# Performance work log

Measured on AMD Instinct MI355X. Metric: run time of the kernel, lower is better.

Reference implementation:

```python
import jax, jax.numpy as jnp
import numpy as np

T, B, E, H = 4096, 1, 256, 8
D = E // H  # head_dim = 32


def setup_inputs() -> dict:
    root = jax.random.key(0)
    ks = jax.random.split(root, 12)
    s = 0.02
    return {
        "query": jax.random.normal(ks[0], (T, B, E), dtype=jnp.float32),
        "key": jax.random.normal(ks[1], (T, B, E), dtype=jnp.float32),
        "value": jax.random.normal(ks[2], (T, B, E), dtype=jnp.float32),
        "residual_attn": jax.random.normal(ks[3], (H, T, T), dtype=jnp.float32),
        "Wq": jax.random.normal(ks[4], (E, E), dtype=jnp.float32) * s,
        "bq": jnp.zeros((E,), dtype=jnp.float32),
        "Wk": jax.random.normal(ks[5], (E, E), dtype=jnp.float32) * s,
        "bk": jnp.zeros((E,), dtype=jnp.float32),
        "Wv": jax.random.normal(ks[6], (E, E), dtype=jnp.float32) * s,
        "bv": jnp.zeros((E,), dtype=jnp.float32),
        "Wo": jax.random.normal(ks[7], (E, E), dtype=jnp.float32) * s,
        "bo": jnp.zeros((E,), dtype=jnp.float32),
    }


def reference(query, key, value, residual_attn, Wq, bq, Wk, bk, Wv, bv, Wo, bo):
    t, b, e = query.shape
    h = H
    d = e // h
    scaling = d ** (-0.5)
    # Original forward: `query = key = self.with_pos_embed(query, pos)` with pos=None,
    # so both q and k are projected from `query`; the `key` arg is ignored.
    qk_src = query
    q = (qk_src @ Wq.T + bq) * scaling          # [T, B, E]
    k = qk_src @ Wk.T + bk                       # [T, B, E]
    v = value @ Wv.T + bv                        # [T, B, E]

    def split_heads(x):
        # [T, B, E] -> [B, H, T, D]
        return x.reshape(t, b, h, d).transpose(1, 2, 0, 3)

    qh, kh, vh = split_heads(q), split_heads(k), split_heads(v)
    # scores: [B, H, T, S] with residual attention added pre-softmax
    scores = jnp.einsum('bhtd,bhsd->bhts', qh, kh) + residual_attn[None]
    attn = jax.nn.softmax(scores, axis=-1)       # dropout p=0.0 -> no-op
    out = jnp.einsum('bhts,bhsd->bhtd', attn, vh)  # [B, H, T, D]
    out = out.transpose(2, 0, 1, 3).reshape(t, b, e)  # [T, B, E]
    return out @ Wo.T + bo
```

## Files before the change

### kernel.cpp

```cpp
#include <hip/hip_runtime.h>
#include <hip/hip_bf16.h>

#define T_DIM 4096
#define E_DIM 256
#define H_DIM 8
#define D_DIM 32
#define SSPLIT 2

typedef __attribute__((ext_vector_type(8))) short short8;
typedef __attribute__((ext_vector_type(4))) float f32x4;

__device__ __forceinline__ unsigned short f2bf(float f) {
    union { float f; unsigned u; } x; x.f = f;
    return (unsigned short)((x.u + 0x7FFFu + ((x.u >> 16) & 1u)) >> 16);
}

struct CastArgs {
    const float* src[6];
    unsigned short* dst[6];
    int n4[6];
};

__global__ __launch_bounds__(256) void cast_kernel(CastArgs a) {
    int b = blockIdx.y;
    const float* s = a.src[b];
    unsigned short* d = a.dst[b];
    int n4 = a.n4[b];
    int i = blockIdx.x * 256 + threadIdx.x;
    if (i < n4) {
        float4 v = reinterpret_cast<const float4*>(s)[i];
        ushort4 o;
        o.x = f2bf(v.x); o.y = f2bf(v.y); o.z = f2bf(v.z); o.w = f2bf(v.w);
        reinterpret_cast<ushort4*>(d)[i] = o;
    }
}

__global__ __launch_bounds__(256) void proj_kernel(
    const unsigned short* __restrict__ qb, const unsigned short* __restrict__ vb,
    const unsigned short* __restrict__ wq, const unsigned short* __restrict__ wk,
    const unsigned short* __restrict__ wv,
    const float* __restrict__ bq, const float* __restrict__ bk, const float* __restrict__ bv,
    unsigned short* __restrict__ qw, unsigned short* __restrict__ kw,
    unsigned short* __restrict__ vt)
{
    const int z = blockIdx.z;
    const unsigned short* A = (z == 2) ? vb : qb;
    const unsigned short* W = (z == 0) ? wq : (z == 1) ? wk : wv;
    const float* bias = (z == 0) ? bq : (z == 1) ? bk : bv;

    const int tid = threadIdx.x;
    const int w = tid >> 6, lane = tid & 63;
    const int g = lane >> 4, r = lane & 15;
    const int t0 = blockIdx.x * 64 + w * 16;
    const int e0 = blockIdx.y * 64;

    f32x4 acc[4];
    const f32x4 zero = {0.f, 0.f, 0.f, 0.f};
    for (int i = 0; i < 4; i++) acc[i] = zero;

    for (int k0 = 0; k0 < E_DIM; k0 += 32) {
        short8 af = *(const short8*)(A + (size_t)(t0 + r) * E_DIM + k0 + g * 8);
        for (int et = 0; et < 4; et++) {
            short8 bf = *(const short8*)(W + (size_t)(e0 + et * 16 + r) * E_DIM + k0 + g * 8);
            acc[et] = __builtin_amdgcn_mfma_f32_16x16x32_bf16(af, bf, acc[et], 0, 0, 0);
        }
    }

    if (z < 2) {
        const float scale = (z == 0) ? 0.17677669529663687f : 1.0f;
        unsigned short* out = (z == 0) ? qw : kw;
        for (int et = 0; et < 4; et++) {
            int e = e0 + et * 16 + r;
            float b = bias[e];
            for (int j = 0; j < 4; j++) {
                int t = t0 + g * 4 + j;
                out[(size_t)t * E_DIM + e] = f2bf((acc[et][j] + b) * scale);
            }
        }
    } else {
        for (int et = 0; et < 4; et++) {
            int e = e0 + et * 16 + r;
            float b = bias[e];
            ushort4 pk;
            pk.x = f2bf(acc[et][0] + b);
            pk.y = f2bf(acc[et][1] + b);
            pk.z = f2bf(acc[et][2] + b);
            pk.w = f2bf(acc[et][3] + b);
            *(ushort4*)(vt + (size_t)e * T_DIM + t0 + g * 4) = pk;
        }
    }
}

__global__ __launch_bounds__(256, 4) void flash_kernel(
    const unsigned short* __restrict__ qw, const unsigned short* __restrict__ kw,
    const unsigned short* __restrict__ vt, const float* __restrict__ residual,
    float* __restrict__ po, float* __restrict__ pl)
{
    __shared__ __align__(16) unsigned short plds[4][16][72];

    const int tid = threadIdx.x;
    const int w = tid >> 6, lane = tid & 63;
    const int g = lane >> 4, r = lane & 15;
    const int h = blockIdx.y;
    const int q0 = blockIdx.x * 64 + w * 16;
    const int sbeg = blockIdx.z * (T_DIM / SSPLIT);
    const int NT = (T_DIM / SSPLIT) / 64;

    short8 qf = *(const short8*)(qw + (size_t)(q0 + r) * E_DIM + h * D_DIM + g * 8);

    const f32x4 zero = {0.f, 0.f, 0.f, 0.f};
    f32x4 oacc[2]; oacc[0] = zero; oacc[1] = zero;
    float lsum = 0.f;

    const float* resptr = residual + (size_t)h * T_DIM * T_DIM
                        + (size_t)(q0 + r) * T_DIM + sbeg + g * 4;
    const unsigned short* kptr = kw + (size_t)(sbeg + r) * E_DIM + h * D_DIM + g * 8;
    const unsigned short* vptr = vt + (size_t)(h * D_DIM + r) * T_DIM + sbeg + g * 8;

    float4 resn[4];
    #pragma unroll
    for (int st = 0; st < 4; st++) resn[st] = *(const float4*)(resptr + st * 16);

    for (int t = 0; t < NT; t++) {
        float4 res[4];
        #pragma unroll
        for (int st = 0; st < 4; st++) res[st] = resn[st];
        if (t + 1 < NT) {
            const float* rp = resptr + (size_t)(t + 1) * 64;
            #pragma unroll
            for (int st = 0; st < 4; st++) resn[st] = *(const float4*)(rp + st * 16);
        }

        short8 kf[4];
        #pragma unroll
        for (int st = 0; st < 4; st++)
            kf[st] = *(const short8*)(kptr + (size_t)(t * 64 + st * 16) * E_DIM);
        short8 vf[2][2];
        #pragma unroll
        for (int dh = 0; dh < 2; dh++)
            #pragma unroll
            for (int sf = 0; sf < 2; sf++)
                vf[dh][sf] = *(const short8*)(vptr + (size_t)dh * 16 * T_DIM + t * 64 + sf * 32);

        #pragma unroll
        for (int st = 0; st < 4; st++) {
            f32x4 sT = __builtin_amdgcn_mfma_f32_16x16x32_bf16(kf[st], qf, zero, 0, 0, 0);
            float p0 = __expf(sT[0] + res[st].x); lsum += p0;
            float p1 = __expf(sT[1] + res[st].y); lsum += p1;
            float p2 = __expf(sT[2] + res[st].z); lsum += p2;
            float p3 = __expf(sT[3] + res[st].w); lsum += p3;
            ushort4 pk;
            pk.x = f2bf(p0); pk.y = f2bf(p1); pk.z = f2bf(p2); pk.w = f2bf(p3);
            *(ushort4*)(&plds[w][r][st * 16 + g * 4]) = pk;
        }

        short8 pa0 = *(const short8*)(&plds[w][r][g * 8]);
        short8 pa1 = *(const short8*)(&plds[w][r][32 + g * 8]);

        oacc[0] = __builtin_amdgcn_mfma_f32_16x16x32_bf16(vf[0][0], pa0, oacc[0], 0, 0, 0);
        oacc[0] = __builtin_amdgcn_mfma_f32_16x16x32_bf16(vf[0][1], pa1, oacc[0], 0, 0, 0);
        oacc[1] = __builtin_amdgcn_mfma_f32_16x16x32_bf16(vf[1][0], pa0, oacc[1], 0, 0, 0);
        oacc[1] = __builtin_amdgcn_mfma_f32_16x16x32_bf16(vf[1][1], pa1, oacc[1], 0, 0, 0);
    }

    lsum += __shfl_xor(lsum, 16);
    lsum += __shfl_xor(lsum, 32);

    float* pob = po + ((size_t)blockIdx.z * H_DIM + h) * T_DIM * D_DIM;
    #pragma unroll
    for (int dh = 0; dh < 2; dh++) {
        float4 ov;
        ov.x = oacc[dh][0]; ov.y = oacc[dh][1]; ov.z = oacc[dh][2]; ov.w = oacc[dh][3];
        *(float4*)(pob + (size_t)(q0 + r) * D_DIM + dh * 16 + g * 4) = ov;
    }
    if (g == 0)
        pl[((size_t)blockIdx.z * H_DIM + h) * T_DIM + q0 + r] = lsum;
}

__global__ __launch_bounds__(256) void combine_kernel(
    const float* __restrict__ po, const float* __restrict__ pl,
    unsigned short* __restrict__ attn)
{
    int idx = blockIdx.x * 256 + threadIdx.x;
    int idx4 = idx * 4;
    int t = idx4 / E_DIM;
    int e = idx4 % E_DIM;
    int h = e >> 5, d = e & 31;

    const size_t chunk = (size_t)H_DIM * T_DIM * D_DIM;
    const float* p0 = po + ((size_t)h * T_DIM + t) * D_DIM + d;
    float l = pl[(size_t)h * T_DIM + t] + pl[(size_t)(H_DIM + h) * T_DIM + t];
    float rl = 1.0f / l;

    float4 a = *(const float4*)p0;
    float4 b = *(const float4*)(p0 + chunk);
    ushort4 o;
    o.x = f2bf((a.x + b.x) * rl);
    o.y = f2bf((a.y + b.y) * rl);
    o.z = f2bf((a.z + b.z) * rl);
    o.w = f2bf((a.w + b.w) * rl);
    *(ushort4*)(attn + (size_t)t * E_DIM + e) = o;
}

__global__ __launch_bounds__(256) void oproj_kernel(
    const unsigned short* __restrict__ attn, const unsigned short* __restrict__ wo,
    const float* __restrict__ bo, float* __restrict__ out)
{
    const int tid = threadIdx.x;
    const int w = tid >> 6, lane = tid & 63;
    const int g = lane >> 4, r = lane & 15;
    const int t0 = blockIdx.x * 64 + w * 16;
    const int e0 = blockIdx.y * 64;

    f32x4 acc[4];
    const f32x4 zero = {0.f, 0.f, 0.f, 0.f};
    for (int i = 0; i < 4; i++) acc[i] = zero;

    for (int k0 = 0; k0 < E_DIM; k0 += 32) {
        short8 af = *(const short8*)(attn + (size_t)(t0 + r) * E_DIM + k0 + g * 8);
        for (int et = 0; et < 4; et++) {
            short8 bf = *(const short8*)(wo + (size_t)(e0 + et * 16 + r) * E_DIM + k0 + g * 8);
            acc[et] = __builtin_amdgcn_mfma_f32_16x16x32_bf16(af, bf, acc[et], 0, 0, 0);
        }
    }

    for (int et = 0; et < 4; et++) {
        int e = e0 + et * 16 + r;
        float b = bo[e];
        for (int j = 0; j < 4; j++) {
            int t = t0 + g * 4 + j;
            out[(size_t)t * E_DIM + e] = acc[et][j] + b;
        }
    }
}

extern "C" void kernel_launch(void* const* d_in, const int* in_sizes, int n_in,
                              void* d_out, int out_size, void* d_ws, size_t ws_size,
                              hipStream_t stream)
{
    const float* query    = (const float*)d_in[0];
    const float* value    = (const float*)d_in[2];
    const float* residual = (const float*)d_in[3];
    const float* Wq = (const float*)d_in[4];
    const float* bq = (const float*)d_in[5];
    const float* Wk = (const float*)d_in[6];
    const float* bk = (const float*)d_in[7];
    const float* Wv = (const float*)d_in[8];
    const float* bv = (const float*)d_in[9];
    const float* Wo = (const float*)d_in[10];
    const float* bo = (const float*)d_in[11];
    float* out = (float*)d_out;

    char* ws = (char*)d_ws;
    size_t off = 0;
    auto alloc = [&](size_t bytes) -> char* {
        char* p = ws + off;
        off = (off + bytes + 255) & ~(size_t)255;
        return p;
    };
    const size_t TE = (size_t)T_DIM * E_DIM;
    const size_t EE = (size_t)E_DIM * E_DIM;

    unsigned short* qb  = (unsigned short*)alloc(TE * 2);
    unsigned short* vb  = (unsigned short*)alloc(TE * 2);
    unsigned short* wqc = (unsigned short*)alloc(EE * 2);
    unsigned short* wkc = (unsigned short*)alloc(EE * 2);
    unsigned short* wvc = (unsigned short*)alloc(EE * 2);
    unsigned short* woc = (unsigned short*)alloc(EE * 2);
    unsigned short* qwp = (unsigned short*)alloc(TE * 2);
    unsigned short* kwp = (unsigned short*)alloc(TE * 2);
    unsigned short* vtp = (unsigned short*)alloc(TE * 2);
    unsigned short* attn = (unsigned short*)alloc(TE * 2);
    float* po = (float*)alloc((size_t)SSPLIT * H_DIM * T_DIM * D_DIM * 4);
    float* pl = (float*)alloc((size_t)SSPLIT * H_DIM * T_DIM * 4);

    CastArgs ca;
    ca.src[0] = query; ca.dst[0] = qb;  ca.n4[0] = (int)(TE / 4);
    ca.src[1] = value; ca.dst[1] = vb;  ca.n4[1] = (int)(TE / 4);
    ca.src[2] = Wq;    ca.dst[2] = wqc; ca.n4[2] = (int)(EE / 4);
    ca.src[3] = Wk;    ca.dst[3] = wkc; ca.n4[3] = (int)(EE / 4);
    ca.src[4] = Wv;    ca.dst[4] = wvc; ca.n4[4] = (int)(EE / 4);
    ca.src[5] = Wo;    ca.dst[5] = woc; ca.n4[5] = (int)(EE / 4);

    dim3 cgrid((unsigned)((TE / 4 + 255) / 256), 6);
    hipLaunchKernelGGL(cast_kernel, cgrid, dim3(256), 0, stream, ca);

    proj_kernel<<<dim3(T_DIM / 64, E_DIM / 64, 3), 256, 0, stream>>>(
        qb, vb, wqc, wkc, wvc, bq, bk, bv, qwp, kwp, vtp);

    flash_kernel<<<dim3(T_DIM / 64, H_DIM, SSPLIT), 256, 0, stream>>>(
        qwp, kwp, vtp, residual, po, pl);

    combine_kernel<<<dim3((unsigned)(TE / 4 / 256)), 256, 0, stream>>>(po, pl, attn);

    oproj_kernel<<<dim3(T_DIM / 64, E_DIM / 64), 256, 0, stream>>>(attn, woc, bo, out);
}
```

Before: 814.5 us.

## Fuse split combine into output projection and batch residual loads per 128 keys

The attention kernel now loads eight residual float4 values up front for each 128-key window and processes them as two 64-key sub-tiles, in place of software-prefetching the next 64-key tile. K and V loads move inside each sub-tile. The separate combine kernel is removed: the output projection kernel now reads both split partial outputs and row sums, normalizes and converts to bf16 on the fly, which saves one launch and a bf16 round trip through memory. In exchange, each of the four column blocks of the projection rereads the fp32 partials, and the residual stream loses explicit cross-iteration prefetch.

```diff
diff --git a/kernel.cpp b/kernel.cpp
--- a/kernel.cpp
+++ b/kernel.cpp
@@ -104,7 +104,7 @@
     const int h = blockIdx.y;
     const int q0 = blockIdx.x * 64 + w * 16;
     const int sbeg = blockIdx.z * (T_DIM / SSPLIT);
-    const int NT = (T_DIM / SSPLIT) / 64;
+    const int NW = (T_DIM / SSPLIT) / 128;
 
     short8 qf = *(const short8*)(qw + (size_t)(q0 + r) * E_DIM + h * D_DIM + g * 8);
 
@@ -112,55 +112,53 @@
     f32x4 oacc[2]; oacc[0] = zero; oacc[1] = zero;
     float lsum = 0.f;
 
-    const float* resptr = residual + (size_t)h * T_DIM * T_DIM
-                        + (size_t)(q0 + r) * T_DIM + sbeg + g * 4;
-    const unsigned short* kptr = kw + (size_t)(sbeg + r) * E_DIM + h * D_DIM + g * 8;
-    const unsigned short* vptr = vt + (size_t)(h * D_DIM + r) * T_DIM + sbeg + g * 8;
-
-    float4 resn[4];
-    #pragma unroll
-    for (int st = 0; st < 4; st++) resn[st] = *(const float4*)(resptr + st * 16);
-
-    for (int t = 0; t < NT; t++) {
-        float4 res[4];
+    const float* resrow = residual + (size_t)h * T_DIM * T_DIM
+                        + (size_t)(q0 + r) * T_DIM + g * 4;
+    const unsigned short* kbase = kw + (size_t)(sbeg + r) * E_DIM + h * D_DIM + g * 8;
+    const unsigned short* vbase = vt + (size_t)(h * D_DIM + r) * T_DIM + sbeg + g * 8;
+
+    for (int it = 0; it < NW; it++) {
+        const int s0 = sbeg + it * 128;
+        const int srel = it * 128;
+
+        float4 rw[8];
         #pragma unroll
-        for (int st = 0; st < 4; st++) res[st] = resn[st];
-        if (t + 1 < NT) {
-            const float* rp = resptr + (size_t)(t + 1) * 64;
+        for (int c = 0; c < 8; c++)
+            rw[c] = *(const float4*)(resrow + s0 + c * 16);
+
+        #pragma unroll
+        for (int u = 0; u < 2; u++) {
+            short8 kf[4];
             #pragma unroll
-            for (int st = 0; st < 4; st++) resn[st] = *(const float4*)(rp + st * 16);
-        }
-
-        short8 kf[4];
-        #pragma unroll
-        for (int st = 0; st < 4; st++)
-            kf[st] = *(const short8*)(kptr + (size_t)(t * 64 + st * 16) * E_DIM);
-        short8 vf[2][2];
-        #pragma unroll
-        for (int dh = 0; dh < 2; dh++)
+            for (int st = 0; st < 4; st++)
+                kf[st] = *(const short8*)(kbase + (size_t)(srel + u * 64 + st * 16) * E_DIM);
+
             #pragma unroll
-            for (int sf = 0; sf < 2; sf++)
-                vf[dh][sf] = *(const short8*)(vptr + (size_t)dh * 16 * T_DIM + t * 64 + sf * 32);
-
-        #pragma unroll
-        for (int st = 0; st < 4; st++) {
-            f32x4 sT = __builtin_amdgcn_mfma_f32_16x16x32_bf16(kf[st], qf, zero, 0, 0, 0);
-            float p0 = __expf(sT[0] + res[st].x); lsum += p0;
-            float p1 = __expf(sT[1] + res[st].y); lsum += p1;
-            float p2 = __expf(sT[2] + res[st].z); lsum += p2;
-            float p3 = __expf(sT[3] + res[st].w); lsum += p3;
-            ushort4 pk;
-            pk.x = f2bf(p0); pk.y = f2bf(p1); pk.z = f2bf(p2); pk.w = f2bf(p3);
-            *(ushort4*)(&plds[w][r][st * 16 + g * 4]) = pk;
-        }
-
-        short8 pa0 = *(const short8*)(&plds[w][r][g * 8]);
-        short8 pa1 = *(const short8*)(&plds[w][r][32 + g * 8]);
-
-        oacc[0] = __builtin_amdgcn_mfma_f32_16x16x32_bf16(vf[0][0], pa0, oacc[0], 0, 0, 0);
-        oacc[0] = __builtin_amdgcn_mfma_f32_16x16x32_bf16(vf[0][1], pa1, oacc[0], 0, 0, 0);
-        oacc[1] = __builtin_amdgcn_mfma_f32_16x16x32_bf16(vf[1][0], pa0, oacc[1], 0, 0, 0);
-        oacc[1] = __builtin_amdgcn_mfma_f32_16x16x32_bf16(vf[1][1], pa1, oacc[1], 0, 0, 0);
+            for (int st = 0; st < 4; st++) {
+                f32x4 sT = __builtin_amdgcn_mfma_f32_16x16x32_bf16(kf[st], qf, zero, 0, 0, 0);
+                const int c = u * 4 + st;
+                float p0 = __expf(sT[0] + rw[c].x); lsum += p0;
+                float p1 = __expf(sT[1] + rw[c].y); lsum += p1;
+                float p2 = __expf(sT[2] + rw[c].z); lsum += p2;
+                float p3 = __expf(sT[3] + rw[c].w); lsum += p3;
+                ushort4 pk;
+                pk.x = f2bf(p0); pk.y = f2bf(p1); pk.z = f2bf(p2); pk.w = f2bf(p3);
+                *(ushort4*)(&plds[w][r][st * 16 + g * 4]) = pk;
+            }
+
+            short8 pa0 = *(const short8*)(&plds[w][r][g * 8]);
+            short8 pa1 = *(const short8*)(&plds[w][r][32 + g * 8]);
+
+            short8 vf00 = *(const short8*)(vbase + srel + u * 64);
+            short8 vf01 = *(const short8*)(vbase + srel + u * 64 + 32);
+            short8 vf10 = *(const short8*)(vbase + (size_t)16 * T_DIM + srel + u * 64);
+            short8 vf11 = *(const short8*)(vbase + (size_t)16 * T_DIM + srel + u * 64 + 32);
+
+            oacc[0] = __builtin_amdgcn_mfma_f32_16x16x32_bf16(vf00, pa0, oacc[0], 0, 0, 0);
+            oacc[0] = __builtin_amdgcn_mfma_f32_16x16x32_bf16(vf01, pa1, oacc[0], 0, 0, 0);
+            oacc[1] = __builtin_amdgcn_mfma_f32_16x16x32_bf16(vf10, pa0, oacc[1], 0, 0, 0);
+            oacc[1] = __builtin_amdgcn_mfma_f32_16x16x32_bf16(vf11, pa1, oacc[1], 0, 0, 0);
+        }
     }
 
     lsum += __shfl_xor(lsum, 16);
@@ -177,47 +175,49 @@
         pl[((size_t)blockIdx.z * H_DIM + h) * T_DIM + q0 + r] = lsum;
 }
 
-__global__ __launch_bounds__(256) void combine_kernel(
+__global__ __launch_bounds__(256) void oproj_kernel(
     const float* __restrict__ po, const float* __restrict__ pl,
-    unsigned short* __restrict__ attn)
-{
-    int idx = blockIdx.x * 256 + threadIdx.x;
-    int idx4 = idx * 4;
-    int t = idx4 / E_DIM;
-    int e = idx4 % E_DIM;
-    int h = e >> 5, d = e & 31;
-
-    const size_t chunk = (size_t)H_DIM * T_DIM * D_DIM;
-    const float* p0 = po + ((size_t)h * T_DIM + t) * D_DIM + d;
-    float l = pl[(size_t)h * T_DIM + t] + pl[(size_t)(H_DIM + h) * T_DIM + t];
-    float rl = 1.0f / l;
-
-    float4 a = *(const float4*)p0;
-    float4 b = *(const float4*)(p0 + chunk);
-    ushort4 o;
-    o.x = f2bf((a.x + b.x) * rl);
-    o.y = f2bf((a.y + b.y) * rl);
-    o.z = f2bf((a.z + b.z) * rl);
-    o.w = f2bf((a.w + b.w) * rl);
-    *(ushort4*)(attn + (size_t)t * E_DIM + e) = o;
-}
-
-__global__ __launch_bounds__(256) void oproj_kernel(
-    const unsigned short* __restrict__ attn, const unsigned short* __restrict__ wo,
-    const float* __restrict__ bo, float* __restrict__ out)
+    const unsigned short* __restrict__ wo, const float* __restrict__ bo,
+    float* __restrict__ out)
 {
     const int tid = threadIdx.x;
     const int w = tid >> 6, lane = tid & 63;
     const int g = lane >> 4, r = lane & 15;
     const int t0 = blockIdx.x * 64 + w * 16;
     const int e0 = blockIdx.y * 64;
+    const int t = t0 + r;
+    const size_t chunk = (size_t)H_DIM * T_DIM * D_DIM;
+
+    float lrec[8];
+    #pragma unroll
+    for (int hh = 0; hh < 8; hh++)
+        lrec[hh] = 1.0f / (pl[(size_t)hh * T_DIM + t] + pl[(size_t)(H_DIM + hh) * T_DIM + t]);
 
     f32x4 acc[4];
     const f32x4 zero = {0.f, 0.f, 0.f, 0.f};
     for (int i = 0; i < 4; i++) acc[i] = zero;
 
+    #pragma unroll
     for (int k0 = 0; k0 < E_DIM; k0 += 32) {
-        short8 af = *(const short8*)(attn + (size_t)(t0 + r) * E_DIM + k0 + g * 8);
+        const int hh = k0 >> 5;
+        const float* pp = po + ((size_t)hh * T_DIM + t) * D_DIM + g * 8;
+        float4 a0 = *(const float4*)(pp);
+        float4 a1 = *(const float4*)(pp + 4);
+        float4 b0 = *(const float4*)(pp + chunk);
+        float4 b1 = *(const float4*)(pp + chunk + 4);
+        const float rl = lrec[hh];
+
+        short8 af;
+        af[0] = (short)f2bf((a0.x + b0.x) * rl);
+        af[1] = (short)f2bf((a0.y + b0.y) * rl);
+        af[2] = (short)f2bf((a0.z + b0.z) * rl);
+        af[3] = (short)f2bf((a0.w + b0.w) * rl);
+        af[4] = (short)f2bf((a1.x + b1.x) * rl);
+        af[5] = (short)f2bf((a1.y + b1.y) * rl);
+        af[6] = (short)f2bf((a1.z + b1.z) * rl);
+        af[7] = (short)f2bf((a1.w + b1.w) * rl);
+
+        #pragma unroll
         for (int et = 0; et < 4; et++) {
             short8 bf = *(const short8*)(wo + (size_t)(e0 + et * 16 + r) * E_DIM + k0 + g * 8);
             acc[et] = __builtin_amdgcn_mfma_f32_16x16x32_bf16(af, bf, acc[et], 0, 0, 0);
@@ -228,8 +228,8 @@
         int e = e0 + et * 16 + r;
         float b = bo[e];
         for (int j = 0; j < 4; j++) {
-            int t = t0 + g * 4 + j;
-            out[(size_t)t * E_DIM + e] = acc[et][j] + b;
+            int tt = t0 + g * 4 + j;
+            out[(size_t)tt * E_DIM + e] = acc[et][j] + b;
         }
     }
 }
@@ -270,7 +270,6 @@
     unsigned short* qwp = (unsigned short*)alloc(TE * 2);
     unsigned short* kwp = (unsigned short*)alloc(TE * 2);
     unsigned short* vtp = (unsigned short*)alloc(TE * 2);
-    unsigned short* attn = (unsigned short*)alloc(TE * 2);
     float* po = (float*)alloc((size_t)SSPLIT * H_DIM * T_DIM * D_DIM * 4);
     float* pl = (float*)alloc((size_t)SSPLIT * H_DIM * T_DIM * 4);
 
@@ -291,7 +290,5 @@
     flash_kernel<<<dim3(T_DIM / 64, H_DIM, SSPLIT), 256, 0, stream>>>(
         qwp, kwp, vtp, residual, po, pl);
 
-    combine_kernel<<<dim3((unsigned)(TE / 4 / 256)), 256, 0, stream>>>(po, pl, attn);
-
-    oproj_kernel<<<dim3(T_DIM / 64, E_DIM / 64), 256, 0, stream>>>(attn, woc, bo, out);
-}
+    oproj_kernel<<<dim3(T_DIM / 64, E_DIM / 64), 256, 0, stream>>>(po, pl, woc, bo, out);
+}
```

After: 818.1 us. About the same (+0.4%).
